# Optimization experiments

Measured on AMD Instinct MI355X. Metric: run time of the kernel, lower is better.

The kernel has to match this reference:

```python
import jax, jax.numpy as jnp
import numpy as np

N = 100000
E = 1600000
IN_C = 128
HID = 128
NUM_CLASSES = 10


def setup_inputs() -> dict:
    key = jax.random.key(0)
    k1, k2, k3, k4 = jax.random.split(key, 4)
    x = jax.random.normal(k1, (N, IN_C), dtype=jnp.float32)
    edge_index = jax.random.randint(k2, (2, E), 0, N, dtype=jnp.int64)
    # PyG Linear weights are [out, in]; glorot-ish scale
    W1 = jax.random.normal(k3, (HID, IN_C), dtype=jnp.float32) / np.sqrt(IN_C)
    b1 = jnp.zeros((HID,), dtype=jnp.float32)
    W2 = jax.random.normal(k4, (NUM_CLASSES, HID), dtype=jnp.float32) / np.sqrt(HID)
    b2 = jnp.zeros((NUM_CLASSES,), dtype=jnp.float32)
    return {"x": x, "edge_index": edge_index, "W1": W1, "b1": b1, "W2": W2, "b2": b2}


def _gcn_conv(x, W, b, row, col, n):
    """Faithful PyG GCNConv: linear transform, symmetric gcn_norm with self-loops,
    gather-scale-scatter aggregation, then bias."""
    h = x @ W.T  # [N, out]
    # add self loops
    loop = jnp.arange(n, dtype=row.dtype)
    r = jnp.concatenate([row, loop])
    c = jnp.concatenate([col, loop])
    # degree at destination (col), edge weight = 1
    deg = jax.ops.segment_sum(jnp.ones(r.shape[0], dtype=h.dtype), c, num_segments=n)
    dis = jnp.where(deg > 0, jax.lax.rsqrt(deg), 0.0)
    norm = dis[r] * dis[c]  # [E+N]
    msgs = norm[:, None] * h[r]  # gather + scale, [E+N, out]
    out = jax.ops.segment_sum(msgs, c, num_segments=n)  # scatter-add
    return out + b


def reference(x, edge_index, W1, b1, W2, b2):
    row, col = edge_index[0], edge_index[1]
    n = x.shape[0]
    x = _gcn_conv(x, W1, b1, row, col, n)
    x = _gcn_conv(x, W2, b2, row, col, n)
    return x
```

## Files before the change

kernel.cpp:

```cpp
#include <hip/hip_runtime.h>
#include <hip/hip_fp16.h>

#define N_NODES 100000
#define E_EDGES 1600000
#define NCLS 10

#define BW 256
#define NB 391
#define EPB 8192
#define NBLK_BIN 196

__global__ __launch_bounds__(256) void k_hist(const int* __restrict__ col,
                                              int* __restrict__ blockHist) {
    __shared__ int h[NB];
    int t = threadIdx.x;
    for (int i = t; i < NB; i += 256) h[i] = 0;
    __syncthreads();
    int base = blockIdx.x * EPB;
    int end  = min(base + EPB, E_EDGES);
    for (int e = base + t; e < end; e += 256)
        atomicAdd(&h[col[e] >> 8], 1);
    __syncthreads();
    for (int i = t; i < NB; i += 256)
        blockHist[blockIdx.x * NB + i] = h[i];
}

__global__ __launch_bounds__(512) void k_scan_w12(int* __restrict__ blockHist,
                                                  int* __restrict__ bucketBase,
                                                  const float* __restrict__ W1,
                                                  const float* __restrict__ W2,
                                                  const float* __restrict__ b1,
                                                  float* __restrict__ W12,
                                                  float* __restrict__ c1) {
    __shared__ int   s[512];
    __shared__ float w2s[1280];
    int t = threadIdx.x;
    if (blockIdx.x == 0) {
        int run = 0;
        if (t < NB) {
            for (int b = 0; b < NBLK_BIN; ++b) {
                int v = blockHist[b * NB + t];
                blockHist[b * NB + t] = run;
                run += v;
            }
        }
        s[t] = (t < NB) ? run : 0;
        __syncthreads();
        for (int st = 1; st < 512; st <<= 1) {
            int tmp = (t >= st) ? s[t - st] : 0;
            __syncthreads();
            s[t] += tmp;
            __syncthreads();
        }
        if (t < NB) bucketBase[t] = s[t] - run;
        if (t == NB - 1) bucketBase[NB] = s[t];
    } else {
        for (int i = t; i < 1280; i += 512) w2s[i] = W2[i];
        __syncthreads();
        if (t < 128) {
            float acc[NCLS];
            #pragma unroll
            for (int j = 0; j < NCLS; ++j) acc[j] = 0.f;
            for (int m = 0; m < 128; ++m) {
                float w1mk = W1[m * 128 + t];
                #pragma unroll
                for (int j = 0; j < NCLS; ++j) acc[j] += w2s[j * 128 + m] * w1mk;
            }
            #pragma unroll
            for (int j = 0; j < NCLS; ++j) W12[j * 128 + t] = acc[j];
        } else if (t < 144) {
            int j = t - 128;
            float acc = 0.f;
            if (j < NCLS)
                for (int m = 0; m < 128; ++m) acc += W2[j * 128 + m] * b1[m];
            c1[j] = (j < NCLS) ? acc : 0.f;
        }
    }
}

__global__ __launch_bounds__(256) void k_bin(const int* __restrict__ ei,
                                             const int* __restrict__ blockHist,
                                             const int* __restrict__ bucketBase,
                                             unsigned* __restrict__ binned) {
    __shared__ int h[NB];
    __shared__ int chunk[NB];
    int t = threadIdx.x;
    for (int i = t; i < NB; i += 256) {
        h[i] = 0;
        chunk[i] = bucketBase[i] + blockHist[blockIdx.x * NB + i];
    }
    __syncthreads();
    int base = blockIdx.x * EPB;
    int end  = min(base + EPB, E_EDGES);
    const int* col = ei + E_EDGES;
    for (int e = base + t; e < end; e += 256) {
        int c = col[e];
        int r = ei[e];
        int k = c >> 8;
        int slot = chunk[k] + atomicAdd(&h[k], 1);
        binned[slot] = ((unsigned)r << 8) | (unsigned)(c & 255);
    }
}

__global__ __launch_bounds__(256) void k_build(const unsigned* __restrict__ binned,
                                               const int* __restrict__ bucketBase,
                                               int* __restrict__ degi,
                                               int* __restrict__ offs,
                                               float* __restrict__ dis,
                                               int* __restrict__ csr) {
    __shared__ int cnt[BW];
    __shared__ int sc[BW];
    __shared__ int eoff[BW];
    __shared__ int cur[BW];
    int k = blockIdx.x;
    int t = threadIdx.x;
    cnt[t] = 0;
    __syncthreads();
    int s0 = bucketBase[k], s1 = bucketBase[k + 1];
    for (int i = s0 + t; i < s1; i += 256)
        atomicAdd(&cnt[binned[i] & 255], 1);
    __syncthreads();
    int v = cnt[t];
    sc[t] = v;
    __syncthreads();
    for (int st = 1; st < 256; st <<= 1) {
        int tmp = (t >= st) ? sc[t - st] : 0;
        __syncthreads();
        sc[t] += tmp;
        __syncthreads();
    }
    eoff[t] = sc[t] - v;
    cur[t] = 0;
    int node = k * BW + t;
    if (node < N_NODES) {
        degi[node] = v;
        offs[node] = s0 + eoff[t];
        dis[node]  = rsqrtf((float)(v + 1));
    }
    __syncthreads();
    for (int i = s0 + t; i < s1; i += 256) {
        unsigned p = binned[i];
        int lc = p & 255;
        int r  = p >> 8;
        int pos = s0 + eoff[lc] + atomicAdd(&cur[lc], 1);
        csr[pos] = r;
    }
}

__global__ __launch_bounds__(64) void k_g1(const float* __restrict__ x,
                                           const float* __restrict__ dis,
                                           const float* __restrict__ W12,
                                           __half2* __restrict__ g1h) {
    int row = blockIdx.x * 64 + threadIdx.x;
    if (row >= N_NODES) return;

    const float4* x4 = (const float4*)x;
    float acc[NCLS];
    #pragma unroll
    for (int j = 0; j < NCLS; ++j) acc[j] = 0.f;

    #pragma unroll
    for (int k4 = 0; k4 < 32; ++k4) {
        float4 xv = x4[row * 32 + k4];
        #pragma unroll
        for (int j = 0; j < NCLS; ++j) {
            const float* wj = &W12[j * 128 + k4 * 4];
            acc[j] += xv.x * wj[0] + xv.y * wj[1] + xv.z * wj[2] + xv.w * wj[3];
        }
    }

    float d = dis[row];
    __half2 hp[8];
    #pragma unroll
    for (int j = 0; j < 5; ++j)
        hp[j] = __floats2half2_rn(d * acc[2 * j], d * acc[2 * j + 1]);
    hp[5] = __floats2half2_rn(0.f, 0.f);
    hp[6] = hp[5];
    hp[7] = hp[5];
    uint4* dst = (uint4*)&g1h[row * 8];
    dst[0] = *(const uint4*)&hp[0];
    dst[1] = *(const uint4*)&hp[4];
}

__global__ __launch_bounds__(256) void k_agg_a(const __half2* __restrict__ g1h,
                                               const float* __restrict__ dis,
                                               const int* __restrict__ csr,
                                               const int* __restrict__ offs,
                                               const int* __restrict__ degi,
                                               const float* __restrict__ c1,
                                               __half2* __restrict__ h2h) {
    int c = blockIdx.x * 32 + (threadIdx.x >> 3);
    int j = threadIdx.x & 7;
    if (c >= N_NODES) return;

    float2 acc = __half22float2(g1h[c * 8 + j]);

    int start = offs[c];
    int deg   = degi[c];
    int k = 0;
    for (; k + 4 <= deg; k += 4) {
        int r0 = csr[start + k + 0];
        int r1 = csr[start + k + 1];
        int r2 = csr[start + k + 2];
        int r3 = csr[start + k + 3];
        float2 a0 = __half22float2(g1h[r0 * 8 + j]);
        float2 a1 = __half22float2(g1h[r1 * 8 + j]);
        float2 a2 = __half22float2(g1h[r2 * 8 + j]);
        float2 a3 = __half22float2(g1h[r3 * 8 + j]);
        acc.x += (a0.x + a1.x) + (a2.x + a3.x);
        acc.y += (a0.y + a1.y) + (a2.y + a3.y);
    }
    for (; k < deg; ++k) {
        float2 a = __half22float2(g1h[csr[start + k] * 8 + j]);
        acc.x += a.x;
        acc.y += a.y;
    }

    float dc = dis[c];
    float ox = dc * (dc * acc.x + c1[2 * j]);
    float oy = dc * (dc * acc.y + c1[2 * j + 1]);
    h2h[c * 8 + j] = __floats2half2_rn(ox, oy);
}

__global__ __launch_bounds__(256) void k_agg_b(const __half2* __restrict__ h2h,
                                               const float* __restrict__ dis,
                                               const int* __restrict__ csr,
                                               const int* __restrict__ offs,
                                               const int* __restrict__ degi,
                                               const float* __restrict__ b2,
                                               float* __restrict__ out) {
    int c = blockIdx.x * 32 + (threadIdx.x >> 3);
    int j = threadIdx.x & 7;
    if (c >= N_NODES) return;

    float2 acc = __half22float2(h2h[c * 8 + j]);

    int start = offs[c];
    int deg   = degi[c];
    int k = 0;
    for (; k + 4 <= deg; k += 4) {
        int r0 = csr[start + k + 0];
        int r1 = csr[start + k + 1];
        int r2 = csr[start + k + 2];
        int r3 = csr[start + k + 3];
        float2 a0 = __half22float2(h2h[r0 * 8 + j]);
        float2 a1 = __half22float2(h2h[r1 * 8 + j]);
        float2 a2 = __half22float2(h2h[r2 * 8 + j]);
        float2 a3 = __half22float2(h2h[r3 * 8 + j]);
        acc.x += (a0.x + a1.x) + (a2.x + a3.x);
        acc.y += (a0.y + a1.y) + (a2.y + a3.y);
    }
    for (; k < deg; ++k) {
        float2 a = __half22float2(h2h[csr[start + k] * 8 + j]);
        acc.x += a.x;
        acc.y += a.y;
    }

    if (j < 5) {
        float dc = dis[c];
        float2 o;
        o.x = dc * acc.x + b2[2 * j];
        o.y = dc * acc.y + b2[2 * j + 1];
        *(float2*)&out[c * NCLS + 2 * j] = o;
    }
}

extern "C" void kernel_launch(void* const* d_in, const int* in_sizes, int n_in,
                              void* d_out, int out_size, void* d_ws, size_t ws_size,
                              hipStream_t stream) {
    const float* x  = (const float*)d_in[0];
    const int*   ei = (const int*)d_in[1];
    const float* W1 = (const float*)d_in[2];
    const float* b1 = (const float*)d_in[3];
    const float* W2 = (const float*)d_in[4];
    const float* b2 = (const float*)d_in[5];
    float* out = (float*)d_out;

    char* ws = (char*)d_ws;
    int*      bucketBase = (int*)(ws + 0);
    float*    W12        = (float*)(ws + 4096);
    float*    c1         = (float*)(ws + 16384);
    int*      blockHist  = (int*)(ws + 32768);
    int*      degi       = (int*)(ws + (1 << 20));
    int*      offs       = (int*)(ws + (2 << 20));
    float*    dis        = (float*)(ws + (3 << 20));
    unsigned* binned     = (unsigned*)(ws + (4 << 20));
    int*      csr        = (int*)(ws + (12 << 20));
    __half2*  g1h        = (__half2*)(ws + (20 << 20));
    __half2*  h2h        = (__half2*)(ws + (24 << 20));

    k_hist<<<NBLK_BIN, 256, 0, stream>>>(ei + E_EDGES, blockHist);
    k_scan_w12<<<2, 512, 0, stream>>>(blockHist, bucketBase, W1, W2, b1, W12, c1);
    k_bin<<<NBLK_BIN, 256, 0, stream>>>(ei, blockHist, bucketBase, binned);
    k_build<<<NB, 256, 0, stream>>>(binned, bucketBase, degi, offs, dis, csr);

    k_g1<<<(N_NODES + 63) / 64, 64, 0, stream>>>(x, dis, W12, g1h);

    k_agg_a<<<(N_NODES + 31) / 32, 256, 0, stream>>>(g1h, dis, csr, offs, degi, c1, h2h);
    k_agg_b<<<(N_NODES + 31) / 32, 256, 0, stream>>>(h2h, dis, csr, offs, degi, b2, out);
}
```

Baseline: 113.9 us.

## Fuse feature projection into CSR build and software-pipeline neighbor index loads

Moves the per-node x·W12 projection into k_build, so the degree-derived scale is applied inside the same kernel and one launch plus the dis reload go away. Offsets and degrees are packed into a single int2 array so each aggregation thread issues one load instead of two. The aggregation loops prefetch the next four CSR indices while gathering the current four, to overlap index latency with the feature gathers. The trade-off is that k_build now runs a 128-wide dot product per thread, which raises its register pressure and puts the x stream in the same kernel as the CSR scatter.

```diff
diff --git a/kernel.cpp b/kernel.cpp
--- a/kernel.cpp
+++ b/kernel.cpp
@@ -104,10 +104,12 @@
 
 __global__ __launch_bounds__(256) void k_build(const unsigned* __restrict__ binned,
                                                const int* __restrict__ bucketBase,
-                                               int* __restrict__ degi,
-                                               int* __restrict__ offs,
+                                               int2* __restrict__ od,
                                                float* __restrict__ dis,
-                                               int* __restrict__ csr) {
+                                               int* __restrict__ csr,
+                                               const float* __restrict__ x,
+                                               const float* __restrict__ W12,
+                                               __half2* __restrict__ g1h) {
     __shared__ int cnt[BW];
     __shared__ int sc[BW];
     __shared__ int eoff[BW];
@@ -132,10 +134,10 @@
     eoff[t] = sc[t] - v;
     cur[t] = 0;
     int node = k * BW + t;
+    float d = rsqrtf((float)(v + 1));
     if (node < N_NODES) {
-        degi[node] = v;
-        offs[node] = s0 + eoff[t];
-        dis[node]  = rsqrtf((float)(v + 1));
+        od[node] = make_int2(s0 + eoff[t], v);
+        dis[node] = d;
     }
     __syncthreads();
     for (int i = s0 + t; i < s1; i += 256) {
@@ -145,48 +147,40 @@
         int pos = s0 + eoff[lc] + atomicAdd(&cur[lc], 1);
         csr[pos] = r;
     }
-}
-
-__global__ __launch_bounds__(64) void k_g1(const float* __restrict__ x,
-                                           const float* __restrict__ dis,
-                                           const float* __restrict__ W12,
-                                           __half2* __restrict__ g1h) {
-    int row = blockIdx.x * 64 + threadIdx.x;
-    if (row >= N_NODES) return;
-
-    const float4* x4 = (const float4*)x;
-    float acc[NCLS];
-    #pragma unroll
-    for (int j = 0; j < NCLS; ++j) acc[j] = 0.f;
-
-    #pragma unroll
-    for (int k4 = 0; k4 < 32; ++k4) {
-        float4 xv = x4[row * 32 + k4];
+
+    if (node < N_NODES) {
+        const float4* x4 = (const float4*)x;
+        float acc[NCLS];
         #pragma unroll
-        for (int j = 0; j < NCLS; ++j) {
-            const float* wj = &W12[j * 128 + k4 * 4];
-            acc[j] += xv.x * wj[0] + xv.y * wj[1] + xv.z * wj[2] + xv.w * wj[3];
-        }
-    }
-
-    float d = dis[row];
-    __half2 hp[8];
-    #pragma unroll
-    for (int j = 0; j < 5; ++j)
-        hp[j] = __floats2half2_rn(d * acc[2 * j], d * acc[2 * j + 1]);
-    hp[5] = __floats2half2_rn(0.f, 0.f);
-    hp[6] = hp[5];
-    hp[7] = hp[5];
-    uint4* dst = (uint4*)&g1h[row * 8];
-    dst[0] = *(const uint4*)&hp[0];
-    dst[1] = *(const uint4*)&hp[4];
+        for (int j = 0; j < NCLS; ++j) acc[j] = 0.f;
+
+        #pragma unroll
+        for (int k4 = 0; k4 < 32; ++k4) {
+            float4 xv = x4[node * 32 + k4];
+            #pragma unroll
+            for (int j = 0; j < NCLS; ++j) {
+                const float* wj = &W12[j * 128 + k4 * 4];
+                acc[j] += xv.x * wj[0] + xv.y * wj[1] + xv.z * wj[2] + xv.w * wj[3];
+            }
+        }
+
+        __half2 hp[8];
+        #pragma unroll
+        for (int j = 0; j < 5; ++j)
+            hp[j] = __floats2half2_rn(d * acc[2 * j], d * acc[2 * j + 1]);
+        hp[5] = __floats2half2_rn(0.f, 0.f);
+        hp[6] = hp[5];
+        hp[7] = hp[5];
+        uint4* dst = (uint4*)&g1h[node * 8];
+        dst[0] = *(const uint4*)&hp[0];
+        dst[1] = *(const uint4*)&hp[4];
+    }
 }
 
 __global__ __launch_bounds__(256) void k_agg_a(const __half2* __restrict__ g1h,
                                                const float* __restrict__ dis,
                                                const int* __restrict__ csr,
-                                               const int* __restrict__ offs,
-                                               const int* __restrict__ degi,
+                                               const int2* __restrict__ od,
                                                const float* __restrict__ c1,
                                                __half2* __restrict__ h2h) {
     int c = blockIdx.x * 32 + (threadIdx.x >> 3);
@@ -195,20 +189,31 @@
 
     float2 acc = __half22float2(g1h[c * 8 + j]);
 
-    int start = offs[c];
-    int deg   = degi[c];
+    int2 odv  = od[c];
+    int start = odv.x;
+    int deg   = odv.y;
     int k = 0;
-    for (; k + 4 <= deg; k += 4) {
-        int r0 = csr[start + k + 0];
-        int r1 = csr[start + k + 1];
-        int r2 = csr[start + k + 2];
-        int r3 = csr[start + k + 3];
-        float2 a0 = __half22float2(g1h[r0 * 8 + j]);
-        float2 a1 = __half22float2(g1h[r1 * 8 + j]);
-        float2 a2 = __half22float2(g1h[r2 * 8 + j]);
-        float2 a3 = __half22float2(g1h[r3 * 8 + j]);
+    if (deg >= 4) {
+        int i0 = csr[start + 0], i1 = csr[start + 1];
+        int i2 = csr[start + 2], i3 = csr[start + 3];
+        for (; k + 8 <= deg; k += 4) {
+            int n0 = csr[start + k + 4], n1 = csr[start + k + 5];
+            int n2 = csr[start + k + 6], n3 = csr[start + k + 7];
+            float2 a0 = __half22float2(g1h[i0 * 8 + j]);
+            float2 a1 = __half22float2(g1h[i1 * 8 + j]);
+            float2 a2 = __half22float2(g1h[i2 * 8 + j]);
+            float2 a3 = __half22float2(g1h[i3 * 8 + j]);
+            acc.x += (a0.x + a1.x) + (a2.x + a3.x);
+            acc.y += (a0.y + a1.y) + (a2.y + a3.y);
+            i0 = n0; i1 = n1; i2 = n2; i3 = n3;
+        }
+        float2 a0 = __half22float2(g1h[i0 * 8 + j]);
+        float2 a1 = __half22float2(g1h[i1 * 8 + j]);
+        float2 a2 = __half22float2(g1h[i2 * 8 + j]);
+        float2 a3 = __half22float2(g1h[i3 * 8 + j]);
         acc.x += (a0.x + a1.x) + (a2.x + a3.x);
         acc.y += (a0.y + a1.y) + (a2.y + a3.y);
+        k += 4;
     }
     for (; k < deg; ++k) {
         float2 a = __half22float2(g1h[csr[start + k] * 8 + j]);
@@ -225,8 +230,7 @@
 __global__ __launch_bounds__(256) void k_agg_b(const __half2* __restrict__ h2h,
                                                const float* __restrict__ dis,
                                                const int* __restrict__ csr,
-                                               const int* __restrict__ offs,
-                                               const int* __restrict__ degi,
+                                               const int2* __restrict__ od,
                                                const float* __restrict__ b2,
                                                float* __restrict__ out) {
     int c = blockIdx.x * 32 + (threadIdx.x >> 3);
@@ -235,20 +239,31 @@
 
     float2 acc = __half22float2(h2h[c * 8 + j]);
 
-    int start = offs[c];
-    int deg   = degi[c];
+    int2 odv  = od[c];
+    int start = odv.x;
+    int deg   = odv.y;
     int k = 0;
-    for (; k + 4 <= deg; k += 4) {
-        int r0 = csr[start + k + 0];
-        int r1 = csr[start + k + 1];
-        int r2 = csr[start + k + 2];
-        int r3 = csr[start + k + 3];
-        float2 a0 = __half22float2(h2h[r0 * 8 + j]);
-        float2 a1 = __half22float2(h2h[r1 * 8 + j]);
-        float2 a2 = __half22float2(h2h[r2 * 8 + j]);
-        float2 a3 = __half22float2(h2h[r3 * 8 + j]);
+    if (deg >= 4) {
+        int i0 = csr[start + 0], i1 = csr[start + 1];
+        int i2 = csr[start + 2], i3 = csr[start + 3];
+        for (; k + 8 <= deg; k += 4) {
+            int n0 = csr[start + k + 4], n1 = csr[start + k + 5];
+            int n2 = csr[start + k + 6], n3 = csr[start + k + 7];
+            float2 a0 = __half22float2(h2h[i0 * 8 + j]);
+            float2 a1 = __half22float2(h2h[i1 * 8 + j]);
+            float2 a2 = __half22float2(h2h[i2 * 8 + j]);
+            float2 a3 = __half22float2(h2h[i3 * 8 + j]);
+            acc.x += (a0.x + a1.x) + (a2.x + a3.x);
+            acc.y += (a0.y + a1.y) + (a2.y + a3.y);
+            i0 = n0; i1 = n1; i2 = n2; i3 = n3;
+        }
+        float2 a0 = __half22float2(h2h[i0 * 8 + j]);
+        float2 a1 = __half22float2(h2h[i1 * 8 + j]);
+        float2 a2 = __half22float2(h2h[i2 * 8 + j]);
+        float2 a3 = __half22float2(h2h[i3 * 8 + j]);
         acc.x += (a0.x + a1.x) + (a2.x + a3.x);
         acc.y += (a0.y + a1.y) + (a2.y + a3.y);
+        k += 4;
     }
     for (; k < deg; ++k) {
         float2 a = __half22float2(h2h[csr[start + k] * 8 + j]);
@@ -281,8 +296,7 @@
     float*    W12        = (float*)(ws + 4096);
     float*    c1         = (float*)(ws + 16384);
     int*      blockHist  = (int*)(ws + 32768);
-    int*      degi       = (int*)(ws + (1 << 20));
-    int*      offs       = (int*)(ws + (2 << 20));
+    int2*     od         = (int2*)(ws + (1 << 20));
     float*    dis        = (float*)(ws + (3 << 20));
     unsigned* binned     = (unsigned*)(ws + (4 << 20));
     int*      csr        = (int*)(ws + (12 << 20));
@@ -292,10 +306,8 @@
     k_hist<<<NBLK_BIN, 256, 0, stream>>>(ei + E_EDGES, blockHist);
     k_scan_w12<<<2, 512, 0, stream>>>(blockHist, bucketBase, W1, W2, b1, W12, c1);
     k_bin<<<NBLK_BIN, 256, 0, stream>>>(ei, blockHist, bucketBase, binned);
-    k_build<<<NB, 256, 0, stream>>>(binned, bucketBase, degi, offs, dis, csr);
-
-    k_g1<<<(N_NODES + 63) / 64, 64, 0, stream>>>(x, dis, W12, g1h);
-
-    k_agg_a<<<(N_NODES + 31) / 32, 256, 0, stream>>>(g1h, dis, csr, offs, degi, c1, h2h);
-    k_agg_b<<<(N_NODES + 31) / 32, 256, 0, stream>>>(h2h, dis, csr, offs, degi, b2, out);
-}
+    k_build<<<NB, 256, 0, stream>>>(binned, bucketBase, od, dis, csr, x, W12, g1h);
+
+    k_agg_a<<<(N_NODES + 31) / 32, 256, 0, stream>>>(g1h, dis, csr, od, c1, h2h);
+    k_agg_b<<<(N_NODES + 31) / 32, 256, 0, stream>>>(h2h, dis, csr, od, b2, out);
+}
```

Result: faster. 105.9 us (-7.0%).
